# Kernel optimization log

Hardware: AMD Instinct MI355X
Metric: run time of the kernel (lower is better)

The kernel has to match this reference:

```python
import jax, jax.numpy as jnp
import numpy as np

WINDOW = 5
SIGMA = 4.0
KSIZE = 2 * int(4.0 * SIGMA + 0.5) + 1  # 33, matches torchvision GaussianBlur setup

H1, W1, B, N, C = 56, 56, 16, 32, 512
PAD = WINDOW - 1


def _gauss_kernel():
    x = jnp.arange(KSIZE, dtype=jnp.float32) - (KSIZE - 1) / 2.0
    k = jnp.exp(-0.5 * (x / SIGMA) ** 2)
    return k / jnp.sum(k)


def _blur(img):
    # separable Gaussian blur with reflect padding (torchvision GaussianBlur default)
    k = _gauss_kernel()
    p = KSIZE // 2
    x = jnp.pad(img, ((0, 0), (0, 0), (p, p), (p, p)), mode='reflect')
    dn = ('NCHW', 'OIHW', 'NCHW')
    x = jax.lax.conv_general_dilated(x, k.reshape(1, 1, KSIZE, 1), (1, 1), 'VALID', dimension_numbers=dn)
    x = jax.lax.conv_general_dilated(x, k.reshape(1, 1, 1, KSIZE), (1, 1), 'VALID', dimension_numbers=dn)
    return x


def _forward(embeddings, memory_bank, out_h, out_w):
    H, W, Bb, Cc = embeddings.shape
    x_norm = jnp.sum(embeddings * embeddings, axis=-1, keepdims=True)  # H W B 1
    best = None
    for d1 in range(WINDOW):
        for d2 in range(WINDOW):
            y = memory_bank[d1:H + d1, d2:W + d2]            # H W N C (shifted slice)
            y_norm = jnp.sum(y * y, axis=-1)                  # H W N
            cross = jnp.einsum('hwbc,hwnc->hwbn', embeddings, y)
            dsq = jnp.maximum(x_norm - 2.0 * cross + y_norm[:, :, None, :], 0.0)
            dmin = jnp.sqrt(jnp.min(dsq, axis=-1))            # H W B
            best = dmin if best is None else jnp.minimum(best, dmin)
    pix = jnp.transpose(best, (2, 0, 1))[:, None, :, :]        # B 1 H W
    img = jnp.max(pix, axis=(1, 2, 3))                         # B
    pix = jax.image.resize(pix, (Bb, 1, out_h, out_w), method='linear')  # align_corners=False bilinear
    return img, _blur(pix)


def setup_inputs() -> dict:
    key = jax.random.key(0)
    k1, k2 = jax.random.split(key)
    embeddings = jax.random.normal(k1, (H1, W1, B, C), dtype=jnp.float32)
    memory_bank = jax.random.normal(k2, (H1 + PAD, W1 + PAD, N, C), dtype=jnp.float32)
    return {'embeddings': embeddings, 'memory_bank': memory_bank, 'out_h': 224, 'out_w': 224}


def reference(embeddings, memory_bank, out_h, out_w):
    return _forward(embeddings, memory_bank, out_h, out_w)
```

## Files before the change

### kernel.cpp

```cpp
#include <hip/hip_runtime.h>
#include <math.h>

#define H1 56
#define W1 56
#define BB 16
#define NN 32
#define CC 512
#define MH 60
#define MW 60
#define OH 224
#define OW 224

typedef __bf16 bf16x8 __attribute__((ext_vector_type(8)));
typedef float floatx4 __attribute__((ext_vector_type(4)));

#define MBH_OFF   0
#define EMBH_OFF  29491200
#define F_XN_OFF  42336256
#define F_YN_OFF  42386432
#define F_BEST_OFF 42501632
#define F_UP_OFF  42551808
#define F_TMP_OFF 43354624
#define F_TOTAL_FLOATS 44157440ull

#define S_XN_OFF   0
#define S_YN_OFF   50176
#define S_BEST_OFF 165376
#define S_UP_OFF   215552
#define S_TMP_OFF  1018368

__global__ void cvt_norm_kernel(const float* __restrict__ src, __bf16* __restrict__ dsth,
                                float* __restrict__ norm, int nvec) {
    int wid  = (int)((blockIdx.x * blockDim.x + threadIdx.x) >> 6);
    int lane = threadIdx.x & 63;
    if (wid >= nvec) return;
    const float* p = src + (size_t)wid * CC + lane * 8;
    floatx4 a = *(const floatx4*)p;
    floatx4 b = *(const floatx4*)(p + 4);
    if (dsth) {
        bf16x8 v;
        v[0] = (__bf16)a.x; v[1] = (__bf16)a.y; v[2] = (__bf16)a.z; v[3] = (__bf16)a.w;
        v[4] = (__bf16)b.x; v[5] = (__bf16)b.y; v[6] = (__bf16)b.z; v[7] = (__bf16)b.w;
        *(bf16x8*)(dsth + (size_t)wid * CC + lane * 8) = v;
    }
    float s = a.x*a.x + a.y*a.y + a.z*a.z + a.w*a.w
            + b.x*b.x + b.y*b.y + b.z*b.z + b.w*b.w;
    s += __shfl_xor(s, 32, 64);
    s += __shfl_xor(s, 16, 64);
    s += __shfl_xor(s, 8, 64);
    s += __shfl_xor(s, 4, 64);
    s += __shfl_xor(s, 2, 64);
    s += __shfl_xor(s, 1, 64);
    if (lane == 0) norm[wid] = s;
}

#define BSTRIDE 520

__global__ __launch_bounds__(256, 4) void dist_kernel_bf16(
        const __bf16* __restrict__ embh, const __bf16* __restrict__ mbh,
        const float* __restrict__ xnorm, const float* __restrict__ ynorm,
        float* __restrict__ best) {
    __shared__ __bf16 Bs[NN * BSTRIDE];

    int bx   = blockIdx.x;
    int h    = bx / 14;
    int w0   = (bx % 14) * 4;
    int tid  = threadIdx.x;
    int wave = tid >> 6;
    int lane = tid & 63;
    int nrow = lane & 15;
    int seg  = lane >> 4;
    int w    = w0 + wave;

    bf16x8 afrag[16];
    const __bf16* ap = embh + ((size_t)(h * W1 + w) * BB + nrow) * CC + seg * 8;
#pragma unroll
    for (int kk = 0; kk < 16; kk++)
        afrag[kk] = *(const bf16x8*)(ap + kk * 32);
    floatx4 xn = *(const floatx4*)(xnorm + (size_t)(h * W1 + w) * BB + seg * 4);

    float bestv[4] = {1e30f, 1e30f, 1e30f, 1e30f};

    for (int d1 = 0; d1 < 5; d1++) {
        int mr = h + d1;
        for (int j = 0; j < 8; j++) {
            int mc = w0 + j;
            const __bf16* bp = mbh + (size_t)(mr * MW + mc) * NN * CC;
            __syncthreads();
#pragma unroll
            for (int t = 0; t < 8; t++) {
                int s  = t * 256 + tid;
                int n  = s >> 6;
                int ch = s & 63;
                *(bf16x8*)(&Bs[n * BSTRIDE + ch * 8]) = *(const bf16x8*)(bp + n * CC + ch * 8);
            }
            __syncthreads();

            int d2 = j - wave;
            if (d2 >= 0 && d2 < 5) {
                float yn0 = ynorm[(size_t)(mr * MW + mc) * NN + nrow];
                float yn1 = ynorm[(size_t)(mr * MW + mc) * NN + nrow + 16];
                floatx4 acc0 = {0.f, 0.f, 0.f, 0.f};
                floatx4 acc1 = {0.f, 0.f, 0.f, 0.f};
#pragma unroll
                for (int kk = 0; kk < 16; kk++) {
                    bf16x8 b0 = *(const bf16x8*)(&Bs[nrow * BSTRIDE + kk * 32 + seg * 8]);
                    bf16x8 b1 = *(const bf16x8*)(&Bs[(nrow + 16) * BSTRIDE + kk * 32 + seg * 8]);
                    acc0 = __builtin_amdgcn_mfma_f32_16x16x32_bf16(afrag[kk], b0, acc0, 0, 0, 0);
                    acc1 = __builtin_amdgcn_mfma_f32_16x16x32_bf16(afrag[kk], b1, acc1, 0, 0, 0);
                }
#pragma unroll
                for (int r = 0; r < 4; r++) {
                    float d0  = fmaxf(xn[r] - 2.f * acc0[r] + yn0, 0.f);
                    float d1v = fmaxf(xn[r] - 2.f * acc1[r] + yn1, 0.f);
                    bestv[r] = fminf(bestv[r], fminf(d0, d1v));
                }
            }
        }
    }

#pragma unroll
    for (int r = 0; r < 4; r++) {
        float v = bestv[r];
        v = fminf(v, __shfl_xor(v, 1, 64));
        v = fminf(v, __shfl_xor(v, 2, 64));
        v = fminf(v, __shfl_xor(v, 4, 64));
        v = fminf(v, __shfl_xor(v, 8, 64));
        bestv[r] = v;
    }
    if ((lane & 15) == 0) {
        int pos = h * W1 + w;
#pragma unroll
        for (int r = 0; r < 4; r++) {
            int b = seg * 4 + r;
            best[(size_t)b * (H1 * W1) + pos] = sqrtf(bestv[r]);
        }
    }
}

__global__ __launch_bounds__(256) void dist_kernel_f32(
        const float* __restrict__ emb, const float* __restrict__ mb,
        const float* __restrict__ xnorm, const float* __restrict__ ynorm,
        float* __restrict__ best) {
    __shared__ __bf16 Bs[NN * BSTRIDE];

    int bx   = blockIdx.x;
    int h    = bx / 14;
    int w0   = (bx % 14) * 4;
    int tid  = threadIdx.x;
    int wave = tid >> 6;
    int lane = tid & 63;
    int nrow = lane & 15;
    int seg  = lane >> 4;
    int w    = w0 + wave;

    bf16x8 afrag[16];
    const float* ap = emb + ((size_t)(h * W1 + w) * BB + nrow) * CC + seg * 8;
#pragma unroll
    for (int kk = 0; kk < 16; kk++) {
        floatx4 f0 = *(const floatx4*)(ap + kk * 32);
        floatx4 f1 = *(const floatx4*)(ap + kk * 32 + 4);
        bf16x8 v;
        v[0] = (__bf16)f0.x; v[1] = (__bf16)f0.y; v[2] = (__bf16)f0.z; v[3] = (__bf16)f0.w;
        v[4] = (__bf16)f1.x; v[5] = (__bf16)f1.y; v[6] = (__bf16)f1.z; v[7] = (__bf16)f1.w;
        afrag[kk] = v;
    }
    floatx4 xn = *(const floatx4*)(xnorm + (size_t)(h * W1 + w) * BB + seg * 4);

    float bestv[4] = {1e30f, 1e30f, 1e30f, 1e30f};

    for (int d1 = 0; d1 < 5; d1++) {
        int mr = h + d1;
        for (int j = 0; j < 8; j++) {
            int mc = w0 + j;
            const float* bp = mb + (size_t)(mr * MW + mc) * NN * CC;
            __syncthreads();
#pragma unroll
            for (int t = 0; t < 8; t++) {
                int c0 = t * 256 + tid;
                int n  = c0 >> 6;
                int ks = (c0 & 63) << 3;
                floatx4 f0 = *(const floatx4*)(bp + n * CC + ks);
                floatx4 f1 = *(const floatx4*)(bp + n * CC + ks + 4);
                bf16x8 v;
                v[0] = (__bf16)f0.x; v[1] = (__bf16)f0.y; v[2] = (__bf16)f0.z; v[3] = (__bf16)f0.w;
                v[4] = (__bf16)f1.x; v[5] = (__bf16)f1.y; v[6] = (__bf16)f1.z; v[7] = (__bf16)f1.w;
                *(bf16x8*)(&Bs[n * BSTRIDE + ks]) = v;
            }
            __syncthreads();

            int d2 = j - wave;
            if (d2 >= 0 && d2 < 5) {
                float yn0 = ynorm[(size_t)(mr * MW + mc) * NN + nrow];
                float yn1 = ynorm[(size_t)(mr * MW + mc) * NN + nrow + 16];
                floatx4 acc0 = {0.f, 0.f, 0.f, 0.f};
                floatx4 acc1 = {0.f, 0.f, 0.f, 0.f};
#pragma unroll
                for (int kk = 0; kk < 16; kk++) {
                    bf16x8 b0 = *(const bf16x8*)(&Bs[nrow * BSTRIDE + kk * 32 + seg * 8]);
                    bf16x8 b1 = *(const bf16x8*)(&Bs[(nrow + 16) * BSTRIDE + kk * 32 + seg * 8]);
                    acc0 = __builtin_amdgcn_mfma_f32_16x16x32_bf16(afrag[kk], b0, acc0, 0, 0, 0);
                    acc1 = __builtin_amdgcn_mfma_f32_16x16x32_bf16(afrag[kk], b1, acc1, 0, 0, 0);
                }
#pragma unroll
                for (int r = 0; r < 4; r++) {
                    float d0  = fmaxf(xn[r] - 2.f * acc0[r] + yn0, 0.f);
                    float d1v = fmaxf(xn[r] - 2.f * acc1[r] + yn1, 0.f);
                    bestv[r] = fminf(bestv[r], fminf(d0, d1v));
                }
            }
        }
    }

#pragma unroll
    for (int r = 0; r < 4; r++) {
        float v = bestv[r];
        v = fminf(v, __shfl_xor(v, 1, 64));
        v = fminf(v, __shfl_xor(v, 2, 64));
        v = fminf(v, __shfl_xor(v, 4, 64));
        v = fminf(v, __shfl_xor(v, 8, 64));
        bestv[r] = v;
    }
    if ((lane & 15) == 0) {
        int pos = h * W1 + w;
#pragma unroll
        for (int r = 0; r < 4; r++) {
            int b = seg * 4 + r;
            best[(size_t)b * (H1 * W1) + pos] = sqrtf(bestv[r]);
        }
    }
}

__global__ void max_kernel(const float* __restrict__ best, float* __restrict__ out) {
    __shared__ float red[256];
    int b = blockIdx.x;
    float m = 0.f;
    for (int i = threadIdx.x; i < H1 * W1; i += 256)
        m = fmaxf(m, best[(size_t)b * (H1 * W1) + i]);
    red[threadIdx.x] = m;
    __syncthreads();
    for (int s = 128; s > 0; s >>= 1) {
        if (threadIdx.x < s) red[threadIdx.x] = fmaxf(red[threadIdx.x], red[threadIdx.x + s]);
        __syncthreads();
    }
    if (threadIdx.x == 0) out[b] = red[0];
}

__global__ void up_kernel(const float* __restrict__ best, float* __restrict__ up) {
    int idx = blockIdx.x * 256 + threadIdx.x;
    int x = idx % OW;
    int y = (idx / OW) % OH;
    int b = idx / (OW * OH);
    const float fr[4] = {0.625f, 0.875f, 0.125f, 0.375f};

    int qy = y >> 2, ry = y & 3;
    int ly = qy + ((ry < 2) ? -1 : 0);
    float ty = fr[ry];
    int hy = min(ly + 1, H1 - 1); ly = max(ly, 0);

    int qx = x >> 2, rx = x & 3;
    int lx = qx + ((rx < 2) ? -1 : 0);
    float tx = fr[rx];
    int hx = min(lx + 1, W1 - 1); lx = max(lx, 0);

    const float* p = best + (size_t)b * (H1 * W1);
    float v00 = p[ly * W1 + lx], v01 = p[ly * W1 + hx];
    float v10 = p[hy * W1 + lx], v11 = p[hy * W1 + hx];
    up[idx] = (1.f - ty) * ((1.f - tx) * v00 + tx * v01)
            + ty * ((1.f - tx) * v10 + tx * v11);
}

struct GaussK { float k[33]; };

__device__ __forceinline__ int refl(int i, int n) {
    i = (i < 0) ? -i : i;
    i = (i > n - 1) ? 2 * (n - 1) - i : i;
    return i;
}

__global__ void blurh_kernel(const float* __restrict__ src, float* __restrict__ dst, GaussK g) {
    int idx = blockIdx.x * 256 + threadIdx.x;
    int x = idx % OW;
    int y = (idx / OW) % OH;
    int b = idx / (OW * OH);
    const float* p = src + (size_t)b * OH * OW;
    float acc = 0.f;
#pragma unroll
    for (int u = 0; u < 33; u++) {
        int yy = refl(y - 16 + u, OH);
        acc += g.k[u] * p[yy * OW + x];
    }
    dst[idx] = acc;
}

__global__ void blurw_kernel(const float* __restrict__ src, float* __restrict__ dst, GaussK g) {
    int idx = blockIdx.x * 256 + threadIdx.x;
    int x = idx % OW;
    int y = (idx / OW) % OH;
    int b = idx / (OW * OH);
    const float* p = src + (size_t)b * OH * OW + (size_t)y * OW;
    float acc = 0.f;
#pragma unroll
    for (int u = 0; u < 33; u++) {
        int xx = refl(x - 16 + u, OW);
        acc += g.k[u] * p[xx];
    }
    dst[idx] = acc;
}

extern "C" void kernel_launch(void* const* d_in, const int* in_sizes, int n_in,
                              void* d_out, int out_size, void* d_ws, size_t ws_size,
                              hipStream_t stream) {
    const float* emb = (const float*)d_in[0];
    const float* mbp = (const float*)d_in[1];
    float* ws  = (float*)d_ws;
    float* out = (float*)d_out;

    bool big = ws_size >= F_TOTAL_FLOATS * 4ull;

    float* xnorm = ws + (big ? F_XN_OFF   : S_XN_OFF);
    float* ynorm = ws + (big ? F_YN_OFF   : S_YN_OFF);
    float* best  = ws + (big ? F_BEST_OFF : S_BEST_OFF);
    float* up    = ws + (big ? F_UP_OFF   : S_UP_OFF);
    float* tmp   = ws + (big ? F_TMP_OFF  : S_TMP_OFF);

    if (big) {
        __bf16* mbh  = (__bf16*)(ws + MBH_OFF);
        __bf16* embh = (__bf16*)(ws + EMBH_OFF);
        cvt_norm_kernel<<<(H1 * W1 * BB) / 4, 256, 0, stream>>>(emb, embh, xnorm, H1 * W1 * BB);
        cvt_norm_kernel<<<(MH * MW * NN) / 4, 256, 0, stream>>>(mbp, mbh, ynorm, MH * MW * NN);
        dist_kernel_bf16<<<H1 * 14, 256, 0, stream>>>(embh, mbh, xnorm, ynorm, best);
    } else {
        cvt_norm_kernel<<<(H1 * W1 * BB) / 4, 256, 0, stream>>>(emb, nullptr, xnorm, H1 * W1 * BB);
        cvt_norm_kernel<<<(MH * MW * NN) / 4, 256, 0, stream>>>(mbp, nullptr, ynorm, MH * MW * NN);
        dist_kernel_f32<<<H1 * 14, 256, 0, stream>>>(emb, mbp, xnorm, ynorm, best);
    }

    max_kernel<<<BB, 256, 0, stream>>>(best, out);
    up_kernel<<<(BB * OH * OW) / 256, 256, 0, stream>>>(best, up);

    GaussK g;
    {
        double wsum = 0.0, wd[33];
        for (int u = 0; u < 33; u++) {
            double xk = (u - 16) / 4.0;
            wd[u] = exp(-0.5 * xk * xk);
            wsum += wd[u];
        }
        for (int u = 0; u < 33; u++) g.k[u] = (float)(wd[u] / wsum);
    }
    blurh_kernel<<<(BB * OH * OW) / 256, 256, 0, stream>>>(up, tmp, g);
    blurw_kernel<<<(BB * OH * OW) / 256, 256, 0, stream>>>(tmp, out + 16, g);
}
```

Before: 582.4 us.

## Process two rows per block in distance kernel; fuse upsample into separable blur

The bf16 distance kernel now computes two adjacent output rows per block. Each staged memory-bank tile is reused for both rows across six bank rows instead of five per single row, which roughly cuts global-to-LDS traffic per output in half. This doubles the A fragments held in registers, so the occupancy hint drops from 4 to 2 blocks. Separately, the bilinear upsample is folded into the separable blur: a vertical pass interpolates from the 56-wide grid and writes a narrow intermediate, and a horizontal pass interpolates on the fly. This removes the full-size upsample buffer and one kernel launch.

```diff
diff --git a/kernel.cpp b/kernel.cpp
--- a/kernel.cpp
+++ b/kernel.cpp
@@ -19,15 +19,13 @@
 #define F_XN_OFF  42336256
 #define F_YN_OFF  42386432
 #define F_BEST_OFF 42501632
-#define F_UP_OFF  42551808
-#define F_TMP_OFF 43354624
+#define F_TMP1_OFF 42551808
 #define F_TOTAL_FLOATS 44157440ull
 
 #define S_XN_OFF   0
 #define S_YN_OFF   50176
 #define S_BEST_OFF 165376
-#define S_UP_OFF   215552
-#define S_TMP_OFF  1018368
+#define S_TMP1_OFF 215552
 
 __global__ void cvt_norm_kernel(const float* __restrict__ src, __bf16* __restrict__ dsth,
                                 float* __restrict__ norm, int nvec) {
@@ -56,12 +54,138 @@
 
 #define BSTRIDE 520
 
-__global__ __launch_bounds__(256, 4) void dist_kernel_bf16(
+__global__ __launch_bounds__(256, 2) void dist_kernel_bf16(
         const __bf16* __restrict__ embh, const __bf16* __restrict__ mbh,
         const float* __restrict__ xnorm, const float* __restrict__ ynorm,
         float* __restrict__ best) {
     __shared__ __bf16 Bs[NN * BSTRIDE];
 
+    int bx   = blockIdx.x;
+    int h0   = (bx / 14) * 2;
+    int w0   = (bx % 14) * 4;
+    int tid  = threadIdx.x;
+    int wave = tid >> 6;
+    int lane = tid & 63;
+    int nrow = lane & 15;
+    int seg  = lane >> 4;
+    int w    = w0 + wave;
+
+    bf16x8 afragA[16], afragB[16];
+    const __bf16* apA = embh + ((size_t)(h0 * W1 + w) * BB + nrow) * CC + seg * 8;
+    const __bf16* apB = embh + ((size_t)((h0 + 1) * W1 + w) * BB + nrow) * CC + seg * 8;
+#pragma unroll
+    for (int kk = 0; kk < 16; kk++) {
+        afragA[kk] = *(const bf16x8*)(apA + kk * 32);
+        afragB[kk] = *(const bf16x8*)(apB + kk * 32);
+    }
+    floatx4 xnA = *(const floatx4*)(xnorm + (size_t)(h0 * W1 + w) * BB + seg * 4);
+    floatx4 xnB = *(const floatx4*)(xnorm + (size_t)((h0 + 1) * W1 + w) * BB + seg * 4);
+
+    float bvA[4] = {1e30f, 1e30f, 1e30f, 1e30f};
+    float bvB[4] = {1e30f, 1e30f, 1e30f, 1e30f};
+
+    for (int rr = 0; rr < 6; rr++) {
+        int mr = h0 + rr;
+        for (int j = 0; j < 8; j++) {
+            int mc = w0 + j;
+            const __bf16* bp = mbh + (size_t)(mr * MW + mc) * NN * CC;
+            __syncthreads();
+#pragma unroll
+            for (int t = 0; t < 8; t++) {
+                int s  = t * 256 + tid;
+                int n  = s >> 6;
+                int ch = s & 63;
+                *(bf16x8*)(&Bs[n * BSTRIDE + ch * 8]) = *(const bf16x8*)(bp + n * CC + ch * 8);
+            }
+            __syncthreads();
+
+            int d2 = j - wave;
+            if (d2 >= 0 && d2 < 5) {
+                bool a0 = (rr < 5);
+                bool a1 = (rr >= 1);
+                float yn0 = ynorm[(size_t)(mr * MW + mc) * NN + nrow];
+                float yn1 = ynorm[(size_t)(mr * MW + mc) * NN + nrow + 16];
+                if (a0 && a1) {
+                    floatx4 c0 = {0,0,0,0}, c1 = {0,0,0,0}, c2 = {0,0,0,0}, c3 = {0,0,0,0};
+#pragma unroll
+                    for (int kk = 0; kk < 16; kk++) {
+                        bf16x8 b0 = *(const bf16x8*)(&Bs[nrow * BSTRIDE + kk * 32 + seg * 8]);
+                        bf16x8 b1 = *(const bf16x8*)(&Bs[(nrow + 16) * BSTRIDE + kk * 32 + seg * 8]);
+                        c0 = __builtin_amdgcn_mfma_f32_16x16x32_bf16(afragA[kk], b0, c0, 0, 0, 0);
+                        c1 = __builtin_amdgcn_mfma_f32_16x16x32_bf16(afragA[kk], b1, c1, 0, 0, 0);
+                        c2 = __builtin_amdgcn_mfma_f32_16x16x32_bf16(afragB[kk], b0, c2, 0, 0, 0);
+                        c3 = __builtin_amdgcn_mfma_f32_16x16x32_bf16(afragB[kk], b1, c3, 0, 0, 0);
+                    }
+#pragma unroll
+                    for (int r = 0; r < 4; r++) {
+                        bvA[r] = fminf(bvA[r], fminf(fmaxf(xnA[r] - 2.f * c0[r] + yn0, 0.f),
+                                                     fmaxf(xnA[r] - 2.f * c1[r] + yn1, 0.f)));
+                        bvB[r] = fminf(bvB[r], fminf(fmaxf(xnB[r] - 2.f * c2[r] + yn0, 0.f),
+                                                     fmaxf(xnB[r] - 2.f * c3[r] + yn1, 0.f)));
+                    }
+                } else if (a0) {
+                    floatx4 c0 = {0,0,0,0}, c1 = {0,0,0,0};
+#pragma unroll
+                    for (int kk = 0; kk < 16; kk++) {
+                        bf16x8 b0 = *(const bf16x8*)(&Bs[nrow * BSTRIDE + kk * 32 + seg * 8]);
+                        bf16x8 b1 = *(const bf16x8*)(&Bs[(nrow + 16) * BSTRIDE + kk * 32 + seg * 8]);
+                        c0 = __builtin_amdgcn_mfma_f32_16x16x32_bf16(afragA[kk], b0, c0, 0, 0, 0);
+                        c1 = __builtin_amdgcn_mfma_f32_16x16x32_bf16(afragA[kk], b1, c1, 0, 0, 0);
+                    }
+#pragma unroll
+                    for (int r = 0; r < 4; r++)
+                        bvA[r] = fminf(bvA[r], fminf(fmaxf(xnA[r] - 2.f * c0[r] + yn0, 0.f),
+                                                     fmaxf(xnA[r] - 2.f * c1[r] + yn1, 0.f)));
+                } else {
+                    floatx4 c2 = {0,0,0,0}, c3 = {0,0,0,0};
+#pragma unroll
+                    for (int kk = 0; kk < 16; kk++) {
+                        bf16x8 b0 = *(const bf16x8*)(&Bs[nrow * BSTRIDE + kk * 32 + seg * 8]);
+                        bf16x8 b1 = *(const bf16x8*)(&Bs[(nrow + 16) * BSTRIDE + kk * 32 + seg * 8]);
+                        c2 = __builtin_amdgcn_mfma_f32_16x16x32_bf16(afragB[kk], b0, c2, 0, 0, 0);
+                        c3 = __builtin_amdgcn_mfma_f32_16x16x32_bf16(afragB[kk], b1, c3, 0, 0, 0);
+                    }
+#pragma unroll
+                    for (int r = 0; r < 4; r++)
+                        bvB[r] = fminf(bvB[r], fminf(fmaxf(xnB[r] - 2.f * c2[r] + yn0, 0.f),
+                                                     fmaxf(xnB[r] - 2.f * c3[r] + yn1, 0.f)));
+                }
+            }
+        }
+    }
+
+#pragma unroll
+    for (int r = 0; r < 4; r++) {
+        float v = bvA[r];
+        v = fminf(v, __shfl_xor(v, 1, 64));
+        v = fminf(v, __shfl_xor(v, 2, 64));
+        v = fminf(v, __shfl_xor(v, 4, 64));
+        v = fminf(v, __shfl_xor(v, 8, 64));
+        bvA[r] = v;
+        float u = bvB[r];
+        u = fminf(u, __shfl_xor(u, 1, 64));
+        u = fminf(u, __shfl_xor(u, 2, 64));
+        u = fminf(u, __shfl_xor(u, 4, 64));
+        u = fminf(u, __shfl_xor(u, 8, 64));
+        bvB[r] = u;
+    }
+    if ((lane & 15) == 0) {
+        int posA = h0 * W1 + w;
+        int posB = (h0 + 1) * W1 + w;
+#pragma unroll
+        for (int r = 0; r < 4; r++) {
+            int b = seg * 4 + r;
+            best[(size_t)b * (H1 * W1) + posA] = sqrtf(bvA[r]);
+            best[(size_t)b * (H1 * W1) + posB] = sqrtf(bvB[r]);
+        }
+    }
+}
+
+__global__ __launch_bounds__(256) void dist_kernel_f32(
+        const float* __restrict__ emb, const float* __restrict__ mb,
+        const float* __restrict__ xnorm, const float* __restrict__ ynorm,
+        float* __restrict__ best) {
+    __shared__ __bf16 Bs[NN * BSTRIDE];
     int bx   = blockIdx.x;
     int h    = bx / 14;
     int w0   = (bx % 14) * 4;
@@ -73,88 +197,6 @@
     int w    = w0 + wave;
 
     bf16x8 afrag[16];
-    const __bf16* ap = embh + ((size_t)(h * W1 + w) * BB + nrow) * CC + seg * 8;
-#pragma unroll
-    for (int kk = 0; kk < 16; kk++)
-        afrag[kk] = *(const bf16x8*)(ap + kk * 32);
-    floatx4 xn = *(const floatx4*)(xnorm + (size_t)(h * W1 + w) * BB + seg * 4);
-
-    float bestv[4] = {1e30f, 1e30f, 1e30f, 1e30f};
-
-    for (int d1 = 0; d1 < 5; d1++) {
-        int mr = h + d1;
-        for (int j = 0; j < 8; j++) {
-            int mc = w0 + j;
-            const __bf16* bp = mbh + (size_t)(mr * MW + mc) * NN * CC;
-            __syncthreads();
-#pragma unroll
-            for (int t = 0; t < 8; t++) {
-                int s  = t * 256 + tid;
-                int n  = s >> 6;
-                int ch = s & 63;
-                *(bf16x8*)(&Bs[n * BSTRIDE + ch * 8]) = *(const bf16x8*)(bp + n * CC + ch * 8);
-            }
-            __syncthreads();
-
-            int d2 = j - wave;
-            if (d2 >= 0 && d2 < 5) {
-                float yn0 = ynorm[(size_t)(mr * MW + mc) * NN + nrow];
-                float yn1 = ynorm[(size_t)(mr * MW + mc) * NN + nrow + 16];
-                floatx4 acc0 = {0.f, 0.f, 0.f, 0.f};
-                floatx4 acc1 = {0.f, 0.f, 0.f, 0.f};
-#pragma unroll
-                for (int kk = 0; kk < 16; kk++) {
-                    bf16x8 b0 = *(const bf16x8*)(&Bs[nrow * BSTRIDE + kk * 32 + seg * 8]);
-                    bf16x8 b1 = *(const bf16x8*)(&Bs[(nrow + 16) * BSTRIDE + kk * 32 + seg * 8]);
-                    acc0 = __builtin_amdgcn_mfma_f32_16x16x32_bf16(afrag[kk], b0, acc0, 0, 0, 0);
-                    acc1 = __builtin_amdgcn_mfma_f32_16x16x32_bf16(afrag[kk], b1, acc1, 0, 0, 0);
-                }
-#pragma unroll
-                for (int r = 0; r < 4; r++) {
-                    float d0  = fmaxf(xn[r] - 2.f * acc0[r] + yn0, 0.f);
-                    float d1v = fmaxf(xn[r] - 2.f * acc1[r] + yn1, 0.f);
-                    bestv[r] = fminf(bestv[r], fminf(d0, d1v));
-                }
-            }
-        }
-    }
-
-#pragma unroll
-    for (int r = 0; r < 4; r++) {
-        float v = bestv[r];
-        v = fminf(v, __shfl_xor(v, 1, 64));
-        v = fminf(v, __shfl_xor(v, 2, 64));
-        v = fminf(v, __shfl_xor(v, 4, 64));
-        v = fminf(v, __shfl_xor(v, 8, 64));
-        bestv[r] = v;
-    }
-    if ((lane & 15) == 0) {
-        int pos = h * W1 + w;
-#pragma unroll
-        for (int r = 0; r < 4; r++) {
-            int b = seg * 4 + r;
-            best[(size_t)b * (H1 * W1) + pos] = sqrtf(bestv[r]);
-        }
-    }
-}
-
-__global__ __launch_bounds__(256) void dist_kernel_f32(
-        const float* __restrict__ emb, const float* __restrict__ mb,
-        const float* __restrict__ xnorm, const float* __restrict__ ynorm,
-        float* __restrict__ best) {
-    __shared__ __bf16 Bs[NN * BSTRIDE];
-
-    int bx   = blockIdx.x;
-    int h    = bx / 14;
-    int w0   = (bx % 14) * 4;
-    int tid  = threadIdx.x;
-    int wave = tid >> 6;
-    int lane = tid & 63;
-    int nrow = lane & 15;
-    int seg  = lane >> 4;
-    int w    = w0 + wave;
-
-    bf16x8 afrag[16];
     const float* ap = emb + ((size_t)(h * W1 + w) * BB + nrow) * CC + seg * 8;
 #pragma unroll
     for (int kk = 0; kk < 16; kk++) {
@@ -166,7 +208,6 @@
         afrag[kk] = v;
     }
     floatx4 xn = *(const floatx4*)(xnorm + (size_t)(h * W1 + w) * BB + seg * 4);
-
     float bestv[4] = {1e30f, 1e30f, 1e30f, 1e30f};
 
     for (int d1 = 0; d1 < 5; d1++) {
@@ -193,8 +234,8 @@
             if (d2 >= 0 && d2 < 5) {
                 float yn0 = ynorm[(size_t)(mr * MW + mc) * NN + nrow];
                 float yn1 = ynorm[(size_t)(mr * MW + mc) * NN + nrow + 16];
-                floatx4 acc0 = {0.f, 0.f, 0.f, 0.f};
-                floatx4 acc1 = {0.f, 0.f, 0.f, 0.f};
+                floatx4 acc0 = {0,0,0,0};
+                floatx4 acc1 = {0,0,0,0};
 #pragma unroll
                 for (int kk = 0; kk < 16; kk++) {
                     bf16x8 b0 = *(const bf16x8*)(&Bs[nrow * BSTRIDE + kk * 32 + seg * 8]);
@@ -211,7 +252,6 @@
             }
         }
     }
-
 #pragma unroll
     for (int r = 0; r < 4; r++) {
         float v = bestv[r];
@@ -246,64 +286,50 @@
     if (threadIdx.x == 0) out[b] = red[0];
 }
 
-__global__ void up_kernel(const float* __restrict__ best, float* __restrict__ up) {
+struct GaussK { float k[33]; };
+
+__device__ __forceinline__ int refl(int i, int n) {
+    i = (i < 0) ? -i : i;
+    i = (i > n - 1) ? 2 * (n - 1) - i : i;
+    return i;
+}
+
+__global__ void vblur_kernel(const float* __restrict__ best, float* __restrict__ tmp1, GaussK g) {
+    int idx = blockIdx.x * 256 + threadIdx.x;
+    int lx = idx % W1;
+    int y  = (idx / W1) % OH;
+    int b  = idx / (W1 * OH);
+    const float* p = best + (size_t)b * (H1 * W1);
+    float acc = 0.f;
+#pragma unroll
+    for (int u = 0; u < 33; u++) {
+        int z  = refl(y - 16 + u, OH);
+        int rz = z & 3;
+        float t = 0.125f + 0.25f * (float)((rz + 2) & 3);
+        int lo = (z >> 2) + ((rz < 2) ? -1 : 0);
+        int hi = min(lo + 1, H1 - 1);
+        lo = max(lo, 0);
+        acc += g.k[u] * ((1.f - t) * p[lo * W1 + lx] + t * p[hi * W1 + lx]);
+    }
+    tmp1[idx] = acc;
+}
+
+__global__ void hblur_kernel(const float* __restrict__ tmp1, float* __restrict__ dst, GaussK g) {
     int idx = blockIdx.x * 256 + threadIdx.x;
     int x = idx % OW;
     int y = (idx / OW) % OH;
     int b = idx / (OW * OH);
-    const float fr[4] = {0.625f, 0.875f, 0.125f, 0.375f};
-
-    int qy = y >> 2, ry = y & 3;
-    int ly = qy + ((ry < 2) ? -1 : 0);
-    float ty = fr[ry];
-    int hy = min(ly + 1, H1 - 1); ly = max(ly, 0);
-
-    int qx = x >> 2, rx = x & 3;
-    int lx = qx + ((rx < 2) ? -1 : 0);
-    float tx = fr[rx];
-    int hx = min(lx + 1, W1 - 1); lx = max(lx, 0);
-
-    const float* p = best + (size_t)b * (H1 * W1);
-    float v00 = p[ly * W1 + lx], v01 = p[ly * W1 + hx];
-    float v10 = p[hy * W1 + lx], v11 = p[hy * W1 + hx];
-    up[idx] = (1.f - ty) * ((1.f - tx) * v00 + tx * v01)
-            + ty * ((1.f - tx) * v10 + tx * v11);
-}
-
-struct GaussK { float k[33]; };
-
-__device__ __forceinline__ int refl(int i, int n) {
-    i = (i < 0) ? -i : i;
-    i = (i > n - 1) ? 2 * (n - 1) - i : i;
-    return i;
-}
-
-__global__ void blurh_kernel(const float* __restrict__ src, float* __restrict__ dst, GaussK g) {
-    int idx = blockIdx.x * 256 + threadIdx.x;
-    int x = idx % OW;
-    int y = (idx / OW) % OH;
-    int b = idx / (OW * OH);
-    const float* p = src + (size_t)b * OH * OW;
+    const float* p = tmp1 + ((size_t)b * OH + y) * W1;
     float acc = 0.f;
 #pragma unroll
     for (int u = 0; u < 33; u++) {
-        int yy = refl(y - 16 + u, OH);
-        acc += g.k[u] * p[yy * OW + x];
-    }
-    dst[idx] = acc;
-}
-
-__global__ void blurw_kernel(const float* __restrict__ src, float* __restrict__ dst, GaussK g) {
-    int idx = blockIdx.x * 256 + threadIdx.x;
-    int x = idx % OW;
-    int y = (idx / OW) % OH;
-    int b = idx / (OW * OH);
-    const float* p = src + (size_t)b * OH * OW + (size_t)y * OW;
-    float acc = 0.f;
-#pragma unroll
-    for (int u = 0; u < 33; u++) {
-        int xx = refl(x - 16 + u, OW);
-        acc += g.k[u] * p[xx];
+        int z  = refl(x - 16 + u, OW);
+        int rz = z & 3;
+        float t = 0.125f + 0.25f * (float)((rz + 2) & 3);
+        int lo = (z >> 2) + ((rz < 2) ? -1 : 0);
+        int hi = min(lo + 1, W1 - 1);
+        lo = max(lo, 0);
+        acc += g.k[u] * ((1.f - t) * p[lo] + t * p[hi]);
     }
     dst[idx] = acc;
 }
@@ -321,15 +347,14 @@
     float* xnorm = ws + (big ? F_XN_OFF   : S_XN_OFF);
     float* ynorm = ws + (big ? F_YN_OFF   : S_YN_OFF);
     float* best  = ws + (big ? F_BEST_OFF : S_BEST_OFF);
-    float* up    = ws + (big ? F_UP_OFF   : S_UP_OFF);
-    float* tmp   = ws + (big ? F_TMP_OFF  : S_TMP_OFF);
+    float* tmp1  = ws + (big ? F_TMP1_OFF : S_TMP1_OFF);
 
     if (big) {
         __bf16* mbh  = (__bf16*)(ws + MBH_OFF);
         __bf16* embh = (__bf16*)(ws + EMBH_OFF);
         cvt_norm_kernel<<<(H1 * W1 * BB) / 4, 256, 0, stream>>>(emb, embh, xnorm, H1 * W1 * BB);
         cvt_norm_kernel<<<(MH * MW * NN) / 4, 256, 0, stream>>>(mbp, mbh, ynorm, MH * MW * NN);
-        dist_kernel_bf16<<<H1 * 14, 256, 0, stream>>>(embh, mbh, xnorm, ynorm, best);
+        dist_kernel_bf16<<<28 * 14, 256, 0, stream>>>(embh, mbh, xnorm, ynorm, best);
     } else {
         cvt_norm_kernel<<<(H1 * W1 * BB) / 4, 256, 0, stream>>>(emb, nullptr, xnorm, H1 * W1 * BB);
         cvt_norm_kernel<<<(MH * MW * NN) / 4, 256, 0, stream>>>(mbp, nullptr, ynorm, MH * MW * NN);
@@ -337,7 +362,6 @@
     }
 
     max_kernel<<<BB, 256, 0, stream>>>(best, out);
-    up_kernel<<<(BB * OH * OW) / 256, 256, 0, stream>>>(best, up);
 
     GaussK g;
     {
@@ -349,6 +373,6 @@
         }
         for (int u = 0; u < 33; u++) g.k[u] = (float)(wd[u] / wsum);
     }
-    blurh_kernel<<<(BB * OH * OW) / 256, 256, 0, stream>>>(up, tmp, g);
-    blurw_kernel<<<(BB * OH * OW) / 256, 256, 0, stream>>>(tmp, out + 16, g);
-}
+    vblur_kernel<<<(BB * OH * W1) / 256, 256, 0, stream>>>(best, tmp1, g);
+    hblur_kernel<<<(BB * OH * OW) / 256, 256, 0, stream>>>(tmp1, out + 16, g);
+}
```

Measured after the change: 523.1 us. 1.11x faster.
